# Kernel optimization log

Hardware: AMD Instinct MI355X
Metric: run time of the kernel (lower is better)

The kernel has to match this reference:

```python
import jax, jax.numpy as jnp
import numpy as np

NEG_SLOPE = 0.2
NUM_GRAPHS = 512


def gat_conv(x, W, att_src, att_dst, bias, src, dst, n):
    """Single-head PyG GATConv (concat=True trivially, heads=1).
    x: [N, Fin], W: [Fin, Fout], att_*: [Fout], bias: [Fout].
    src/dst: [E] int32/64 (self-loops already appended).
    """
    h = x @ W                               # [N, Fout]
    a_s = h @ att_src                       # [N]
    a_d = h @ att_dst                       # [N]
    e = a_s[src] + a_d[dst]                 # [E]
    e = jnp.where(e >= 0, e, NEG_SLOPE * e)  # LeakyReLU
    # numerically stable edge-softmax grouped by destination node
    m = jax.ops.segment_max(e, dst, num_segments=n)          # [N]
    w = jnp.exp(e - m[dst])                                   # [E]
    denom = jax.ops.segment_sum(w, dst, num_segments=n)      # [N]
    alpha = w / denom[dst]                                    # [E]
    out = jax.ops.segment_sum(alpha[:, None] * h[src], dst, num_segments=n)
    return out + bias


def setup_inputs() -> dict:
    key = jax.random.key(0)
    ks = jax.random.split(key, 12)
    N, E, FIN, H = 50000, 800000, 768, 64
    x = jax.random.normal(ks[0], (N, FIN), dtype=jnp.float32)
    edge_index = jax.random.randint(ks[1], (2, E), 0, N, dtype=jnp.int64)
    batch = jnp.sort(jax.random.randint(ks[2], (N,), 0, NUM_GRAPHS, dtype=jnp.int64))
    def glorot(k, shape):
        lim = np.sqrt(6.0 / (shape[0] + shape[-1]))
        return jax.random.uniform(k, shape, jnp.float32, -lim, lim)
    return {
        "x": x, "edge_index": edge_index, "batch": batch,
        "W1": glorot(ks[3], (FIN, H)),
        "att_src1": glorot(ks[4], (H,)), "att_dst1": glorot(ks[5], (H,)),
        "b1": jnp.zeros((H,), jnp.float32),
        "W2": glorot(ks[6], (H, H)),
        "att_src2": glorot(ks[7], (H,)), "att_dst2": glorot(ks[8], (H,)),
        "b2": jnp.zeros((H,), jnp.float32),
        "Wlin": glorot(ks[9], (H, 2)),
        "blin": jnp.zeros((2,), jnp.float32),
    }


def reference(x, edge_index, batch, W1, att_src1, att_dst1, b1,
              W2, att_src2, att_dst2, b2, Wlin, blin):
    n = x.shape[0]
    loops = jnp.arange(n, dtype=edge_index.dtype)
    src = jnp.concatenate([edge_index[0], loops])  # add_self_loops=True
    dst = jnp.concatenate([edge_index[1], loops])
    h = gat_conv(x, W1, att_src1, att_dst1, b1, src, dst, n)
    h = jax.nn.relu(h)
    h = gat_conv(h, W2, att_src2, att_dst2, b2, src, dst, n)
    h = jax.nn.relu(h)
    # global_mean_pool
    sums = jax.ops.segment_sum(h, batch, num_segments=NUM_GRAPHS)     # [G, H]
    cnt = jax.ops.segment_sum(jnp.ones((n,), h.dtype), batch, num_segments=NUM_GRAPHS)
    pooled = sums / jnp.maximum(cnt, 1.0)[:, None]
    return pooled @ Wlin + blin
```

## Files before the change

kernel.cpp:

```cpp
#include <hip/hip_runtime.h>

#define NEG_SLOPE 0.2f
#define NGRAPHS 512

typedef short short8 __attribute__((ext_vector_type(8)));
typedef float f32x4 __attribute__((ext_vector_type(4)));

__device__ __forceinline__ float wave_reduce_sum(float v) {
#pragma unroll
    for (int off = 32; off > 0; off >>= 1) v += __shfl_xor(v, off, 64);
    return v;
}
__device__ __forceinline__ float wave_reduce_max(float v) {
#pragma unroll
    for (int off = 32; off > 0; off >>= 1) v = fmaxf(v, __shfl_xor(v, off, 64));
    return v;
}
__device__ __forceinline__ unsigned short f2bf(float f) {
    unsigned u = __float_as_uint(f);
    u += 0x7FFFu + ((u >> 16) & 1u);
    return (unsigned short)(u >> 16);
}

__device__ __forceinline__ void edge_sd(const int* __restrict__ ei, int E, int e,
                                        int& s, int& d) {
    if (e < E) { s = ei[e]; d = ei[E + e]; }
    else { s = d = e - E; }
}

__global__ __launch_bounds__(256) void setup_hist(
    const int* __restrict__ ei, int E, int ET, int* __restrict__ counts,
    int nEdgeBlk, const float* __restrict__ W1, unsigned short* __restrict__ Wt1,
    int K1, const float* __restrict__ W2, unsigned short* __restrict__ Wt2,
    const int* __restrict__ batch, int* __restrict__ gstart, int N) {
    const int b = blockIdx.x, tid = threadIdx.x;
    if (b < nEdgeBlk) {
        int e = b * 256 + tid;
        if (e >= ET) return;
        int s, d;
        edge_sd(ei, E, e, s, d);
        atomicAdd(counts + d, 1);
    } else if (b < nEdgeBlk + 64) {
        int n = b - nEdgeBlk;
        for (int k = tid; k < K1; k += 256)
            Wt1[(size_t)n * K1 + k] = f2bf(W1[(size_t)k * 64 + n]);
    } else if (b == nEdgeBlk + 64) {
#pragma unroll
        for (int i = 0; i < 16; ++i) {
            int idx = tid + i * 256;
            int n = idx >> 6, k = idx & 63;
            Wt2[n * 64 + k] = f2bf(W2[k * 64 + n]);
        }
    } else {
        for (int g = tid; g <= NGRAPHS; g += 256) {
            int lo = 0, hi = N;
            while (lo < hi) {
                int mid = (lo + hi) >> 1;
                if (batch[mid] < g) lo = mid + 1; else hi = mid;
            }
            gstart[g] = lo;
        }
    }
}

__global__ __launch_bounds__(256) void scan_sum(const int* __restrict__ counts,
                                                int* __restrict__ blk_sum, int N,
                                                int CH) {
    __shared__ int wsum[4];
    const int tid = threadIdx.x, lane = tid & 63, wid = tid >> 6;
    const int b = blockIdx.x;
    int begin = b * CH, endi = min(begin + CH, N);
    int s = 0;
    for (int i = begin + tid; i < endi; i += 256) s += counts[i];
#pragma unroll
    for (int off = 32; off > 0; off >>= 1) s += __shfl_xor(s, off, 64);
    if (lane == 0) wsum[wid] = s;
    __syncthreads();
    if (tid == 0) blk_sum[b] = wsum[0] + wsum[1] + wsum[2] + wsum[3];
}

__global__ __launch_bounds__(64) void scan_blk(int* __restrict__ blk_sum,
                                               int* __restrict__ row_ptr, int N,
                                               int nb) {
    int t = threadIdx.x;
    int v = (t < nb) ? blk_sum[t] : 0;
    int sv = v;
#pragma unroll
    for (int off = 1; off < 64; off <<= 1) {
        int u = __shfl_up(sv, off, 64);
        if (t >= off) sv += u;
    }
    if (t < nb) blk_sum[t] = sv - v;
    if (t == nb - 1) row_ptr[N] = sv;
}

__global__ __launch_bounds__(256) void scan_local(const int* __restrict__ counts,
                                                  const int* __restrict__ blk_off,
                                                  int* __restrict__ row_ptr,
                                                  int* __restrict__ next_, int N,
                                                  int CH) {
    __shared__ int wsum[4];
    __shared__ int ctot;
    const int tid = threadIdx.x, lane = tid & 63, wid = tid >> 6;
    const int b = blockIdx.x;
    int begin = b * CH, endi = min(begin + CH, N);
    int carry = blk_off[b];
    for (int base = begin; base < endi; base += 256) {
        int i = base + tid;
        int v = (i < endi) ? counts[i] : 0;
        int sv = v;
#pragma unroll
        for (int off = 1; off < 64; off <<= 1) {
            int u = __shfl_up(sv, off, 64);
            if (lane >= off) sv += u;
        }
        if (lane == 63) wsum[wid] = sv;
        __syncthreads();
        if (tid == 0) {
            int a = 0;
#pragma unroll
            for (int j = 0; j < 4; ++j) { int u = wsum[j]; wsum[j] = a; a += u; }
            ctot = a;
        }
        __syncthreads();
        int excl = carry + wsum[wid] + sv - v;
        if (i < endi) { row_ptr[i] = excl; next_[i] = excl; }
        carry += ctot;
        __syncthreads();
    }
}

__global__ __launch_bounds__(256) void gemm1_fill(
    const float* __restrict__ A, const unsigned short* __restrict__ Wt, int M, int K,
    float* __restrict__ h, const float* __restrict__ att_s,
    const float* __restrict__ att_d, float* __restrict__ a_s,
    float* __restrict__ a_d, int nGemm, const int* __restrict__ ei, int E, int ET,
    int* __restrict__ next_, int* __restrict__ srcs) {
    __shared__ unsigned short As[64][264];
    const int tid = threadIdx.x;
    if (blockIdx.x >= nGemm) {
        int e = (blockIdx.x - nGemm) * 256 + tid;
        if (e >= ET) return;
        int s, d;
        edge_sd(ei, E, e, s, d);
        int pos = atomicAdd(next_ + d, 1);
        srcs[pos] = s;
        return;
    }
    const int w = tid >> 6, l = tid & 63, m = l & 15, q = l >> 4;
    const int row0 = blockIdx.x * 64;
    f32x4 acc0 = {0.f, 0.f, 0.f, 0.f}, acc1 = acc0, acc2 = acc0, acc3 = acc0;
    const int sr = tid >> 2, sc = tid & 3;
    const int grow = row0 + sr;
    const bool rok = grow < M;
    if (!rok) {
#pragma unroll
        for (int u = 0; u < 8; ++u)
            *(uint4*)&As[sr][sc * 64 + u * 8] = make_uint4(0, 0, 0, 0);
    }
    const float* Ap = A + (size_t)grow * K + sc * 64;

    for (int c = 0; c < 3; ++c) {
        if (rok) {
            for (int u = 0; u < 4; ++u) {
                const float4* p = (const float4*)(Ap + c * 256 + u * 16);
                float4 f0 = p[0], f1 = p[1], f2 = p[2], f3 = p[3];
                unsigned short t[16] = {
                    f2bf(f0.x), f2bf(f0.y), f2bf(f0.z), f2bf(f0.w),
                    f2bf(f1.x), f2bf(f1.y), f2bf(f1.z), f2bf(f1.w),
                    f2bf(f2.x), f2bf(f2.y), f2bf(f2.z), f2bf(f2.w),
                    f2bf(f3.x), f2bf(f3.y), f2bf(f3.z), f2bf(f3.w)};
                *(uint4*)&As[sr][sc * 64 + u * 16] = *(uint4*)&t[0];
                *(uint4*)&As[sr][sc * 64 + u * 16 + 8] = *(uint4*)&t[8];
            }
        }
        __syncthreads();
        const unsigned short* arow = &As[w * 16 + m][0];
        const unsigned short* brow = Wt + (size_t)m * K + c * 256;
#pragma unroll
        for (int ks = 0; ks < 8; ++ks) {
            short8 av = *(const short8*)(arow + ks * 32 + q * 8);
            const unsigned short* bp = brow + ks * 32 + q * 8;
            acc0 = __builtin_amdgcn_mfma_f32_16x16x32_bf16(
                av, *(const short8*)(bp), acc0, 0, 0, 0);
            acc1 = __builtin_amdgcn_mfma_f32_16x16x32_bf16(
                av, *(const short8*)(bp + (size_t)16 * K), acc1, 0, 0, 0);
            acc2 = __builtin_amdgcn_mfma_f32_16x16x32_bf16(
                av, *(const short8*)(bp + (size_t)32 * K), acc2, 0, 0, 0);
            acc3 = __builtin_amdgcn_mfma_f32_16x16x32_bf16(
                av, *(const short8*)(bp + (size_t)48 * K), acc3, 0, 0, 0);
        }
        __syncthreads();
    }
    float as0 = att_s[m], as1 = att_s[16 + m], as2 = att_s[32 + m], as3 = att_s[48 + m];
    float ad0 = att_d[m], ad1 = att_d[16 + m], ad2 = att_d[32 + m], ad3 = att_d[48 + m];
    const int rowb = row0 + w * 16 + q * 4;
#pragma unroll
    for (int r = 0; r < 4; ++r) {
        int row = rowb + r;
        float v0 = acc0[r], v1 = acc1[r], v2 = acc2[r], v3 = acc3[r];
        if (row < M) {
            float* hp = h + (size_t)row * 64 + m;
            hp[0] = v0; hp[16] = v1; hp[32] = v2; hp[48] = v3;
        }
        float hs = v0 * as0 + v1 * as1 + v2 * as2 + v3 * as3;
        float hd = v0 * ad0 + v1 * ad1 + v2 * ad2 + v3 * ad3;
#pragma unroll
        for (int off = 1; off < 16; off <<= 1) {
            hs += __shfl_xor(hs, off, 64);
            hd += __shfl_xor(hd, off, 64);
        }
        if (m == 0 && row < M) { a_s[row] = hs; a_d[row] = hd; }
    }
}

__global__ __launch_bounds__(256) void gemm2_mfma(
    const unsigned short* __restrict__ Ab, const unsigned short* __restrict__ Wt2,
    int M, float* __restrict__ h, const float* __restrict__ att_s,
    const float* __restrict__ att_d, float* __restrict__ a_s,
    float* __restrict__ a_d) {
    const int tid = threadIdx.x;
    const int w = tid >> 6, l = tid & 63, m = l & 15, q = l >> 4;
    const int row0 = blockIdx.x * 64;
    const int r = row0 + w * 16 + m;
    short8 av0 = {0, 0, 0, 0, 0, 0, 0, 0}, av1 = av0;
    if (r < M) {
        av0 = *(const short8*)(Ab + (size_t)r * 64 + q * 8);
        av1 = *(const short8*)(Ab + (size_t)r * 64 + 32 + q * 8);
    }
    f32x4 acc0 = {0.f, 0.f, 0.f, 0.f}, acc1 = acc0, acc2 = acc0, acc3 = acc0;
    const unsigned short* bp = Wt2 + (size_t)m * 64 + q * 8;
    acc0 = __builtin_amdgcn_mfma_f32_16x16x32_bf16(av0, *(const short8*)(bp), acc0, 0, 0, 0);
    acc0 = __builtin_amdgcn_mfma_f32_16x16x32_bf16(av1, *(const short8*)(bp + 32), acc0, 0, 0, 0);
    acc1 = __builtin_amdgcn_mfma_f32_16x16x32_bf16(av0, *(const short8*)(bp + 16 * 64), acc1, 0, 0, 0);
    acc1 = __builtin_amdgcn_mfma_f32_16x16x32_bf16(av1, *(const short8*)(bp + 16 * 64 + 32), acc1, 0, 0, 0);
    acc2 = __builtin_amdgcn_mfma_f32_16x16x32_bf16(av0, *(const short8*)(bp + 32 * 64), acc2, 0, 0, 0);
    acc2 = __builtin_amdgcn_mfma_f32_16x16x32_bf16(av1, *(const short8*)(bp + 32 * 64 + 32), acc2, 0, 0, 0);
    acc3 = __builtin_amdgcn_mfma_f32_16x16x32_bf16(av0, *(const short8*)(bp + 48 * 64), acc3, 0, 0, 0);
    acc3 = __builtin_amdgcn_mfma_f32_16x16x32_bf16(av1, *(const short8*)(bp + 48 * 64 + 32), acc3, 0, 0, 0);

    float as0 = att_s[m], as1 = att_s[16 + m], as2 = att_s[32 + m], as3 = att_s[48 + m];
    float ad0 = att_d[m], ad1 = att_d[16 + m], ad2 = att_d[32 + m], ad3 = att_d[48 + m];
    const int rowb = row0 + w * 16 + q * 4;
#pragma unroll
    for (int rr = 0; rr < 4; ++rr) {
        int row = rowb + rr;
        float v0 = acc0[rr], v1 = acc1[rr], v2 = acc2[rr], v3 = acc3[rr];
        if (row < M) {
            float* hp = h + (size_t)row * 64 + m;
            hp[0] = v0; hp[16] = v1; hp[32] = v2; hp[48] = v3;
        }
        float hs = v0 * as0 + v1 * as1 + v2 * as2 + v3 * as3;
        float hd = v0 * ad0 + v1 * ad1 + v2 * ad2 + v3 * ad3;
#pragma unroll
        for (int off = 1; off < 16; off <<= 1) {
            hs += __shfl_xor(hs, off, 64);
            hd += __shfl_xor(hd, off, 64);
        }
        if (m == 0 && row < M) { a_s[row] = hs; a_d[row] = hd; }
    }
}

__global__ __launch_bounds__(256) void gat_agg_kernel(
    const int* __restrict__ row_ptr, const int* __restrict__ srcs,
    const float* __restrict__ a_s, const float* __restrict__ a_d,
    const float* __restrict__ h, const float* __restrict__ bias,
    float* __restrict__ out, unsigned short* __restrict__ outb, int N) {
    int n = blockIdx.x * 4 + (threadIdx.x >> 6);
    int lane = threadIdx.x & 63;
    if (n >= N) return;
    const int start = row_ptr[n];
    const int deg = row_ptr[n + 1] - start;
    const float adn = a_d[n];

    if (deg <= 64) {
        int sl = 0;
        float v = -1e30f;
        if (lane < deg) {
            sl = srcs[start + lane];
            float t = a_s[sl] + adn;
            v = (t >= 0.f) ? t : NEG_SLOPE * t;
        }
        float m = wave_reduce_max(v);
        float wl = (lane < deg) ? __expf(v - m) : 0.f;
        float l = wave_reduce_sum(wl);
        wl *= (1.f / l);

        const int eq = lane >> 4, fq = lane & 15;
        float ax = 0.f, ay = 0.f, az = 0.f, aw = 0.f;
        for (int j = 0; j < deg; j += 4) {
            int idx = j + eq;
            bool ok = idx < deg;
            int ii = ok ? idx : 0;
            float a = __shfl(wl, ii, 64);
            int s = __shfl(sl, ii, 64);
            if (!ok) a = 0.f;
            const float4 hv = *(const float4*)(h + (size_t)s * 64 + fq * 4);
            ax += a * hv.x; ay += a * hv.y; az += a * hv.z; aw += a * hv.w;
        }
#pragma unroll
        for (int off = 16; off <= 32; off <<= 1) {
            ax += __shfl_xor(ax, off, 64);
            ay += __shfl_xor(ay, off, 64);
            az += __shfl_xor(az, off, 64);
            aw += __shfl_xor(aw, off, 64);
        }
        if (eq == 0) {
            const float4 bv = *(const float4*)(bias + fq * 4);
            float4 o;
            o.x = ax + bv.x; o.y = ay + bv.y; o.z = az + bv.z; o.w = aw + bv.w;
            o.x = o.x > 0.f ? o.x : 0.f;
            o.y = o.y > 0.f ? o.y : 0.f;
            o.z = o.z > 0.f ? o.z : 0.f;
            o.w = o.w > 0.f ? o.w : 0.f;
            if (out) *(float4*)(out + (size_t)n * 64 + fq * 4) = o;
            if (outb) {
                unsigned short t[4] = {f2bf(o.x), f2bf(o.y), f2bf(o.z), f2bf(o.w)};
                *(uint2*)(outb + (size_t)n * 64 + fq * 4) = *(uint2*)t;
            }
        }
        return;
    }

    const int end = start + deg;
    float m = -1e30f;
    for (int i = start + lane; i < end; i += 64) {
        float v = a_s[srcs[i]] + adn;
        v = (v >= 0.f) ? v : NEG_SLOPE * v;
        m = fmaxf(m, v);
    }
    m = wave_reduce_max(m);
    float l = 0.f;
    for (int i = start + lane; i < end; i += 64) {
        float v = a_s[srcs[i]] + adn;
        v = (v >= 0.f) ? v : NEG_SLOPE * v;
        l += __expf(v - m);
    }
    l = wave_reduce_sum(l);
    const float inv_den = 1.f / l;
    float acc = 0.f;
    for (int c = start; c < end; c += 64) {
        int cl = end - c;
        if (cl > 64) cl = 64;
        int sl = 0;
        float wl = 0.f;
        if (c + lane < end) {
            sl = srcs[c + lane];
            float v = a_s[sl] + adn;
            v = (v >= 0.f) ? v : NEG_SLOPE * v;
            wl = __expf(v - m) * inv_den;
        }
        for (int j = 0; j < cl; ++j) {
            float wj = __shfl(wl, j, 64);
            int sj = __shfl(sl, j, 64);
            acc += wj * h[(size_t)sj * 64 + lane];
        }
    }
    float o = acc + bias[lane];
    o = o > 0.f ? o : 0.f;
    if (out) out[(size_t)n * 64 + lane] = o;
    if (outb) outb[(size_t)n * 64 + lane] = f2bf(o);
}

__global__ __launch_bounds__(256) void pool_final(const float* __restrict__ x,
                                                  const int* __restrict__ gstart,
                                                  const float* __restrict__ Wlin,
                                                  const float* __restrict__ blin,
                                                  float* __restrict__ out) {
    __shared__ float red[4][64];
    const int g = blockIdx.x;
    const int lane = threadIdx.x & 63, w = threadIdx.x >> 6;
    const int s = gstart[g], e = gstart[g + 1];
    float acc = 0.f;
    for (int n = s + w; n < e; n += 4) acc += x[(size_t)n * 64 + lane];
    red[w][lane] = acc;
    __syncthreads();
    if (w == 0) {
        float p = red[0][lane] + red[1][lane] + red[2][lane] + red[3][lane];
        int c = e - s;
        p /= (float)(c > 1 ? c : 1);
        float o0 = wave_reduce_sum(p * Wlin[lane * 2 + 0]);
        float o1 = wave_reduce_sum(p * Wlin[lane * 2 + 1]);
        if (lane == 0) {
            out[g * 2 + 0] = o0 + blin[0];
            out[g * 2 + 1] = o1 + blin[1];
        }
    }
}

extern "C" void kernel_launch(void* const* d_in, const int* in_sizes, int n_in,
                              void* d_out, int out_size, void* d_ws, size_t ws_size,
                              hipStream_t stream) {
    const float* x    = (const float*)d_in[0];
    const int*   ei   = (const int*)d_in[1];
    const int*   batch= (const int*)d_in[2];
    const float* W1   = (const float*)d_in[3];
    const float* as1  = (const float*)d_in[4];
    const float* ad1  = (const float*)d_in[5];
    const float* b1   = (const float*)d_in[6];
    const float* W2   = (const float*)d_in[7];
    const float* as2  = (const float*)d_in[8];
    const float* ad2  = (const float*)d_in[9];
    const float* b2   = (const float*)d_in[10];
    const float* Wlin = (const float*)d_in[11];
    const float* blin = (const float*)d_in[12];
    float* out = (float*)d_out;

    const int FIN = 768;
    const int N  = in_sizes[0] / FIN;
    const int E  = in_sizes[1] / 2;
    const int ET = E + N;
    const size_t N64 = (size_t)N * 64;
    const int NB = 64;
    const int CH = (N + NB - 1) / NB;

    float* ws     = (float*)d_ws;
    float* hbuf   = ws;
    float* x2     = hbuf + N64;
    float* a_s    = x2 + N64;
    float* a_d    = a_s + N;
    int* counts   = (int*)(a_d + N);
    int* row_ptr  = counts + N;
    int* next     = row_ptr + N + 1;
    int* blk_sum  = next + N;
    int* gstart   = blk_sum + 64;
    int* srcs     = gstart + NGRAPHS + 1;
    uintptr_t wtp = (uintptr_t)(srcs + ET);
    wtp = (wtp + 15) & ~(uintptr_t)15;
    unsigned short* Wt1 = (unsigned short*)wtp;
    unsigned short* Wt2 = Wt1 + (size_t)64 * FIN;
    unsigned short* x1b = Wt2 + (size_t)64 * 64;

    const int nEdgeBlk  = (ET + 255) / 256;
    const int nWaveBlkN = (N + 3) / 4;
    const int nGemmBlk  = (N + 63) / 64;

    hipMemsetAsync(counts, 0, (size_t)N * sizeof(int), stream);

    setup_hist<<<nEdgeBlk + 66, 256, 0, stream>>>(ei, E, ET, counts, nEdgeBlk,
                                                  W1, Wt1, FIN, W2, Wt2,
                                                  batch, gstart, N);
    scan_sum<<<NB, 256, 0, stream>>>(counts, blk_sum, N, CH);
    scan_blk<<<1, 64, 0, stream>>>(blk_sum, row_ptr, N, NB);
    scan_local<<<NB, 256, 0, stream>>>(counts, blk_sum, row_ptr, next, N, CH);

    gemm1_fill<<<nGemmBlk + nEdgeBlk, 256, 0, stream>>>(
        x, Wt1, N, FIN, hbuf, as1, ad1, a_s, a_d, nGemmBlk, ei, E, ET, next, srcs);
    gat_agg_kernel<<<nWaveBlkN, 256, 0, stream>>>(row_ptr, srcs, a_s, a_d, hbuf,
                                                  b1, nullptr, x1b, N);

    gemm2_mfma<<<nGemmBlk, 256, 0, stream>>>(x1b, Wt2, N, hbuf, as2, ad2, a_s, a_d);
    gat_agg_kernel<<<nWaveBlkN, 256, 0, stream>>>(row_ptr, srcs, a_s, a_d, hbuf,
                                                  b2, x2, nullptr, N);

    pool_final<<<NGRAPHS, 256, 0, stream>>>(x2, gstart, Wlin, blin, out);
}
```

Before: 452.0 us.

## Load GEMM1 A operands directly into MFMA registers, dropping LDS staging

The first-layer GEMM no longer stages the fp32 input tile through shared memory with block barriers. Each lane now loads its own 8 fp32 values per k-step straight from global memory, converts them to bf16 and feeds the MFMA directly. The loop is unrolled by 8 and launch bounds now request 4 blocks per CU. This removes the LDS traffic and __syncthreads, but each lane reads only 32 contiguous bytes per row, so global coalescing is weaker and latency hiding depends on the unrolling and occupancy.

```diff
diff --git a/kernel.cpp b/kernel.cpp
--- a/kernel.cpp
+++ b/kernel.cpp
@@ -130,13 +130,12 @@
     }
 }
 
-__global__ __launch_bounds__(256) void gemm1_fill(
+__global__ __launch_bounds__(256, 4) void gemm1_fill(
     const float* __restrict__ A, const unsigned short* __restrict__ Wt, int M, int K,
     float* __restrict__ h, const float* __restrict__ att_s,
     const float* __restrict__ att_d, float* __restrict__ a_s,
     float* __restrict__ a_d, int nGemm, const int* __restrict__ ei, int E, int ET,
     int* __restrict__ next_, int* __restrict__ srcs) {
-    __shared__ unsigned short As[64][264];
     const int tid = threadIdx.x;
     if (blockIdx.x >= nGemm) {
         int e = (blockIdx.x - nGemm) * 256 + tid;
@@ -149,56 +148,38 @@
     }
     const int w = tid >> 6, l = tid & 63, m = l & 15, q = l >> 4;
     const int row0 = blockIdx.x * 64;
+    const int r = row0 + w * 16 + m;
+    const bool rok = r < M;
+    const float* Ap = A + (size_t)r * K + q * 8;
+    const unsigned short* Bp = Wt + (size_t)m * K + q * 8;
     f32x4 acc0 = {0.f, 0.f, 0.f, 0.f}, acc1 = acc0, acc2 = acc0, acc3 = acc0;
-    const int sr = tid >> 2, sc = tid & 3;
-    const int grow = row0 + sr;
-    const bool rok = grow < M;
-    if (!rok) {
-#pragma unroll
-        for (int u = 0; u < 8; ++u)
-            *(uint4*)&As[sr][sc * 64 + u * 8] = make_uint4(0, 0, 0, 0);
-    }
-    const float* Ap = A + (size_t)grow * K + sc * 64;
-
-    for (int c = 0; c < 3; ++c) {
+#pragma unroll 8
+    for (int t = 0; t < 24; ++t) {
+        short8 av = {0, 0, 0, 0, 0, 0, 0, 0};
         if (rok) {
-            for (int u = 0; u < 4; ++u) {
-                const float4* p = (const float4*)(Ap + c * 256 + u * 16);
-                float4 f0 = p[0], f1 = p[1], f2 = p[2], f3 = p[3];
-                unsigned short t[16] = {
-                    f2bf(f0.x), f2bf(f0.y), f2bf(f0.z), f2bf(f0.w),
-                    f2bf(f1.x), f2bf(f1.y), f2bf(f1.z), f2bf(f1.w),
-                    f2bf(f2.x), f2bf(f2.y), f2bf(f2.z), f2bf(f2.w),
-                    f2bf(f3.x), f2bf(f3.y), f2bf(f3.z), f2bf(f3.w)};
-                *(uint4*)&As[sr][sc * 64 + u * 16] = *(uint4*)&t[0];
-                *(uint4*)&As[sr][sc * 64 + u * 16 + 8] = *(uint4*)&t[8];
-            }
-        }
-        __syncthreads();
-        const unsigned short* arow = &As[w * 16 + m][0];
-        const unsigned short* brow = Wt + (size_t)m * K + c * 256;
-#pragma unroll
-        for (int ks = 0; ks < 8; ++ks) {
-            short8 av = *(const short8*)(arow + ks * 32 + q * 8);
-            const unsigned short* bp = brow + ks * 32 + q * 8;
-            acc0 = __builtin_amdgcn_mfma_f32_16x16x32_bf16(
-                av, *(const short8*)(bp), acc0, 0, 0, 0);
-            acc1 = __builtin_amdgcn_mfma_f32_16x16x32_bf16(
-                av, *(const short8*)(bp + (size_t)16 * K), acc1, 0, 0, 0);
-            acc2 = __builtin_amdgcn_mfma_f32_16x16x32_bf16(
-                av, *(const short8*)(bp + (size_t)32 * K), acc2, 0, 0, 0);
-            acc3 = __builtin_amdgcn_mfma_f32_16x16x32_bf16(
-                av, *(const short8*)(bp + (size_t)48 * K), acc3, 0, 0, 0);
-        }
-        __syncthreads();
+            const float4 f0 = *(const float4*)(Ap + t * 32);
+            const float4 f1 = *(const float4*)(Ap + t * 32 + 4);
+            unsigned short tt[8] = {f2bf(f0.x), f2bf(f0.y), f2bf(f0.z), f2bf(f0.w),
+                                    f2bf(f1.x), f2bf(f1.y), f2bf(f1.z), f2bf(f1.w)};
+            av = *(const short8*)tt;
+        }
+        const unsigned short* bp = Bp + t * 32;
+        acc0 = __builtin_amdgcn_mfma_f32_16x16x32_bf16(
+            av, *(const short8*)(bp), acc0, 0, 0, 0);
+        acc1 = __builtin_amdgcn_mfma_f32_16x16x32_bf16(
+            av, *(const short8*)(bp + (size_t)16 * K), acc1, 0, 0, 0);
+        acc2 = __builtin_amdgcn_mfma_f32_16x16x32_bf16(
+            av, *(const short8*)(bp + (size_t)32 * K), acc2, 0, 0, 0);
+        acc3 = __builtin_amdgcn_mfma_f32_16x16x32_bf16(
+            av, *(const short8*)(bp + (size_t)48 * K), acc3, 0, 0, 0);
     }
     float as0 = att_s[m], as1 = att_s[16 + m], as2 = att_s[32 + m], as3 = att_s[48 + m];
     float ad0 = att_d[m], ad1 = att_d[16 + m], ad2 = att_d[32 + m], ad3 = att_d[48 + m];
     const int rowb = row0 + w * 16 + q * 4;
 #pragma unroll
-    for (int r = 0; r < 4; ++r) {
-        int row = rowb + r;
-        float v0 = acc0[r], v1 = acc1[r], v2 = acc2[r], v3 = acc3[r];
+    for (int rr = 0; rr < 4; ++rr) {
+        int row = rowb + rr;
+        float v0 = acc0[rr], v1 = acc1[rr], v2 = acc2[rr], v3 = acc3[rr];
         if (row < M) {
             float* hp = h + (size_t)row * 64 + m;
             hp[0] = v0; hp[16] = v1; hp[32] = v2; hp[48] = v3;
```

Result: no change. 459.2 us (+1.6%).
